# Kernel tuning notes

Measured on AMD Instinct MI355X. Metric: run time of the kernel, lower is better.

## Reference

```python
import jax, jax.numpy as jnp
import numpy as np
import math

H = 2048
NH = 16
NKV = 4
HD = H // NH  # 128
N_REP = NH // NKV
EPS = 1e-6


def rms_norm(x, w, eps=1e-6):
    x32 = x.astype(jnp.float32)
    y = x32 * jax.lax.rsqrt(jnp.mean(x32 * x32, axis=-1, keepdims=True) + eps)
    return (y * w.astype(jnp.float32)).astype(x.dtype)


def mha(normed, key_in, val_in, q_w, k_w, v_w, o_w, bias):
    # normed: [b,s,H]; key_in/val_in: [b,n,H]; bias broadcastable to [b,nh,s,n]
    b, s, _ = normed.shape
    n = key_in.shape[1]
    q = (normed @ q_w).reshape(b, s, NH, HD).transpose(0, 2, 1, 3)      # [b,nh,s,d]
    k = (key_in @ k_w).reshape(b, n, NKV, HD).transpose(0, 2, 1, 3)     # [b,nkv,n,d]
    v = (val_in @ v_w).reshape(b, n, NKV, HD).transpose(0, 2, 1, 3)
    k = jnp.repeat(k, N_REP, axis=1)  # GQA expand -> [b,nh,n,d]
    v = jnp.repeat(v, N_REP, axis=1)
    scores = jnp.einsum('bhsd,bhnd->bhsn', q, k) / math.sqrt(HD) + bias
    probs = jax.nn.softmax(scores.astype(jnp.float32), axis=-1).astype(q.dtype)
    out = jnp.einsum('bhsn,bhnd->bhsd', probs, v)
    out = out.transpose(0, 2, 1, 3).reshape(b, s, NH * HD) @ o_w
    return out, probs


def setup_inputs() -> dict:
    key = jax.random.key(0)
    ks = jax.random.split(key, 20)
    B, S, ND, T = 2, 2048, 64, 2048
    w = lambda k, sh: (jax.random.normal(k, sh, dtype=jnp.float32) * 0.02)
    return {
        'hidden_states': jax.random.normal(ks[0], (B, S, H), dtype=jnp.float32),
        'doc_summary_key': jax.random.normal(ks[1], (B, ND, H), dtype=jnp.float32),
        'doc_summary_value': jax.random.normal(ks[2], (B, ND, H), dtype=jnp.float32),
        'doc_summary_mask': jnp.ones((B, ND), dtype=jnp.float32),
        'token_key': jax.random.normal(ks[3], (B, T, H), dtype=jnp.float32),
        'token_value': jax.random.normal(ks[4], (B, T, H), dtype=jnp.float32),
        'token_mask': jnp.ones((B, T), dtype=jnp.float32),
        'cn_w': jnp.ones((H,), dtype=jnp.float32),
        'cq_w': w(ks[5], (H, NH * HD)),
        'ck_w': w(ks[6], (H, NKV * HD)),
        'cv_w': w(ks[7], (H, NKV * HD)),
        'co_w': w(ks[8], (NH * HD, H)),
        'c_gate': jnp.array([-1.0], dtype=jnp.float32),
        'fn_w': jnp.ones((H,), dtype=jnp.float32),
        'fq_w': w(ks[9], (H, NH * HD)),
        'fk_w': w(ks[10], (H, NKV * HD)),
        'fv_w': w(ks[11], (H, NKV * HD)),
        'fo_w': w(ks[12], (NH * HD, H)),
        'f_gate': jnp.array([-1.0], dtype=jnp.float32),
        'doc_token_map': jax.random.randint(ks[13], (B, T), 0, ND, dtype=jnp.int64)
            if jax.config.jax_enable_x64 else jax.random.randint(ks[13], (B, T), 0, ND).astype(jnp.int32),
    }


def reference(hidden_states, doc_summary_key, doc_summary_value, doc_summary_mask,
              token_key, token_value, token_mask,
              cn_w, cq_w, ck_w, cv_w, co_w, c_gate,
              fn_w, fq_w, fk_w, fv_w, fo_w, f_gate,
              doc_token_map):
    # ---- coarse stage: cross-attention over document summaries ----
    normed = rms_norm(hidden_states, cn_w)
    coarse_bias = ((1.0 - doc_summary_mask) * -1e9)[:, None, None, :]  # [b,1,1,nd]
    attn_out, probs = mha(normed, doc_summary_key, doc_summary_value,
                          cq_w, ck_w, cv_w, co_w, coarse_bias)
    doc_scores = probs.mean(axis=(1, 2))  # [b,nd] avg over heads+query positions
    gate_c = jax.nn.sigmoid(c_gate).astype(attn_out.dtype)
    out = hidden_states + gate_c * attn_out

    # ---- fine stage: cross-attention over token KV with log-doc-score bias ----
    log_ds = jnp.log(doc_scores + EPS)
    doc_bias = jnp.take_along_axis(log_ds, doc_token_map, axis=1)  # [b,T]
    pad_bias = (1.0 - token_mask) * -1e9
    fine_bias = (doc_bias + pad_bias)[:, None, None, :]  # [b,1,1,T]
    normed_f = rms_norm(out, fn_w)
    attn_out_f, _ = mha(normed_f, token_key, token_value,
                        fq_w, fk_w, fv_w, fo_w, fine_bias)
    gate_f = jax.nn.sigmoid(f_gate).astype(attn_out_f.dtype)
    final = out + gate_f * attn_out_f
    return final
```

## Files before the change

### kernel.cpp

```cpp
#include <hip/hip_runtime.h>
#include <hip/hip_bf16.h>

typedef unsigned short u16;
typedef unsigned int u32;
typedef __attribute__((ext_vector_type(8))) short bf16x8;
typedef __attribute__((ext_vector_type(4))) float f32x4;

constexpr int NH = 16;
constexpr int H = 2048;
constexpr float SCALE = 0.08838834764831845f;
constexpr float L2E = 1.4426950408889634f;
constexpr float SCALE2 = SCALE * L2E;
constexpr float THR2 = 8.0f * L2E;

__device__ __forceinline__ u16 f2bf(float f) {
    u32 u = __float_as_uint(f);
    u32 r = u + 0x7fffu + ((u >> 16) & 1u);
    return (u16)(r >> 16);
}
__device__ __forceinline__ u32 pack2(float x, float y) {
    return (u32)f2bf(x) | ((u32)f2bf(y) << 16);
}
__device__ __forceinline__ u32 pack2_cvt(float x, float y) {
    __hip_bfloat162 h = __float22bfloat162_rn(float2{x, y});
    return *reinterpret_cast<u32*>(&h);
}

#define GLD_LDS16(gsrc, ldst)                                                  \
    __builtin_amdgcn_global_load_lds(                                          \
        (const __attribute__((address_space(1))) void*)(gsrc),                 \
        (__attribute__((address_space(3))) void*)(ldst), 16, 0, 0)

__global__ __launch_bounds__(256)
void transpose_cvt4(const float* __restrict__ i0, const float* __restrict__ i1,
                    const float* __restrict__ i2, const float* __restrict__ i3,
                    u16* __restrict__ o0, u16* __restrict__ o1,
                    u16* __restrict__ o2, u16* __restrict__ o3, int K, int N) {
    const float* in = (blockIdx.z == 0) ? i0 : (blockIdx.z == 1) ? i1
                    : (blockIdx.z == 2) ? i2 : i3;
    u16* out = (blockIdx.z == 0) ? o0 : (blockIdx.z == 1) ? o1
             : (blockIdx.z == 2) ? o2 : o3;
    __shared__ u16 tile[32][33];
    int bn = blockIdx.x * 32, bk = blockIdx.y * 32;
    int tx = threadIdx.x & 31, ty = threadIdx.x >> 5;
#pragma unroll
    for (int r = 0; r < 32; r += 8)
        tile[tx][r + ty] = f2bf(in[(size_t)(bk + r + ty) * N + bn + tx]);
    __syncthreads();
#pragma unroll
    for (int r = 0; r < 32; r += 8)
        out[(size_t)(bn + r + ty) * K + bk + tx] = tile[r + ty][tx];
}

__global__ __launch_bounds__(256)
void rmsnorm_cvt(const float* __restrict__ x, const float* __restrict__ w,
                 u16* __restrict__ y, int nrows,
                 const float* __restrict__ ca, u16* __restrict__ coa,
                 const float* __restrict__ cb, u16* __restrict__ cob, int n4) {
    int blk = blockIdx.x;
    int t = threadIdx.x;
    if (blk >= nrows) {
        int nb = gridDim.x - nrows;
        int stride = nb * 256;
        for (int i = (blk - nrows) * 256 + t; i < 2 * n4; i += stride) {
            const float* in;
            u16* out;
            int j = i;
            if (j < n4) { in = ca; out = coa; }
            else { j -= n4; in = cb; out = cob; }
            float4 v = reinterpret_cast<const float4*>(in)[j];
            uint2 o;
            o.x = pack2(v.x, v.y);
            o.y = pack2(v.z, v.w);
            reinterpret_cast<uint2*>(out)[j] = o;
        }
        return;
    }
    int r = blk;
    const float4* xr = reinterpret_cast<const float4*>(x + (size_t)r * H);
    float4 v0 = xr[t * 2], v1 = xr[t * 2 + 1];
    float ss = v0.x * v0.x + v0.y * v0.y + v0.z * v0.z + v0.w * v0.w
             + v1.x * v1.x + v1.y * v1.y + v1.z * v1.z + v1.w * v1.w;
#pragma unroll
    for (int d = 1; d < 64; d <<= 1) ss += __shfl_xor(ss, d);
    __shared__ float red[4];
    if ((t & 63) == 0) red[t >> 6] = ss;
    __syncthreads();
    float tot = red[0] + red[1] + red[2] + red[3];
    float rs = rsqrtf(tot * (1.0f / H) + 1e-6f);
    const float4* wr = reinterpret_cast<const float4*>(w);
    float4 w0 = wr[t * 2], w1 = wr[t * 2 + 1];
    uint4 o;
    o.x = pack2(v0.x * rs * w0.x, v0.y * rs * w0.y);
    o.y = pack2(v0.z * rs * w0.z, v0.w * rs * w0.w);
    o.z = pack2(v1.x * rs * w1.x, v1.y * rs * w1.y);
    o.w = pack2(v1.z * rs * w1.z, v1.w * rs * w1.w);
    reinterpret_cast<uint4*>(y + (size_t)r * H)[t] = o;
}

template <int MODE, int BN>
__device__ __forceinline__
void gemm_body(u16* __restrict__ smem,
               const u16* __restrict__ A, const u16* __restrict__ Bt,
               u16* __restrict__ Cb, float* __restrict__ Cf,
               const float* __restrict__ resid, const float* __restrict__ gate_p,
               int N, int K, int brow, int bcol) {
    constexpr int WN = BN / 32;
    constexpr int BWROWS = BN / 4;
    u16* Asb = smem;
    u16* Bsb = smem + 2 * 128 * 64;
    const int t = threadIdx.x;
    const int lane = t & 63, wid = t >> 6;
    const int wm = wid >> 1, wn = wid & 1;
    const int l15 = lane & 15, hi = lane >> 4;
    const int rsw = l15 & 7;

    f32x4 acc[4][WN] = {};
    const int srow = lane >> 3;
    const int sseg = ((lane & 7) ^ srow) * 8;
    const u16* aBase = A + (size_t)(brow + wid * 32 + srow) * K + sseg;
    const u16* bBase = Bt + (size_t)(bcol + wid * BWROWS + srow) * K + sseg;

#define GSTAGE(KT, BF)                                                          \
    do {                                                                        \
        _Pragma("unroll")                                                       \
        for (int u = 0; u < 4; ++u)                                             \
            GLD_LDS16(aBase + (size_t)(u * 8) * K + (KT),                       \
                      Asb + (BF) * 8192 + (wid * 32 + u * 8) * 64);             \
        _Pragma("unroll")                                                       \
        for (int u = 0; u < BWROWS / 8; ++u)                                    \
            GLD_LDS16(bBase + (size_t)(u * 8) * K + (KT),                       \
                      Bsb + (BF) * (BN * 64) + (wid * BWROWS + u * 8) * 64);    \
    } while (0)

    GSTAGE(0, 0);
    __syncthreads();
    int buf = 0;
    for (int kt = 0; kt < K; kt += 64) {
        if (kt + 64 < K) GSTAGE(kt + 64, buf ^ 1);
        const u16* as = Asb + buf * 8192;
        const u16* bs = Bsb + buf * (BN * 64);
        bf16x8 af[4][2], bfr[WN][2];
#pragma unroll
        for (int i = 0; i < 4; ++i) {
            int row = wm * 64 + i * 16 + l15;
#pragma unroll
            for (int ko = 0; ko < 2; ++ko)
                af[i][ko] = *reinterpret_cast<const bf16x8*>(
                    &as[row * 64 + (((ko * 4 + hi) ^ rsw) * 8)]);
        }
#pragma unroll
        for (int j = 0; j < WN; ++j) {
            int row = wn * (BN / 2) + j * 16 + l15;
#pragma unroll
            for (int ko = 0; ko < 2; ++ko)
                bfr[j][ko] = *reinterpret_cast<const bf16x8*>(
                    &bs[row * 64 + (((ko * 4 + hi) ^ rsw) * 8)]);
        }
#pragma unroll
        for (int ko = 0; ko < 2; ++ko)
#pragma unroll
            for (int i = 0; i < 4; ++i)
#pragma unroll
                for (int j = 0; j < WN; ++j)
                    acc[i][j] = __builtin_amdgcn_mfma_f32_16x16x32_bf16(
                        af[i][ko], bfr[j][ko], acc[i][j], 0, 0, 0);
        __syncthreads();
        buf ^= 1;
    }
#undef GSTAGE

    float g = 0.f;
    if (MODE == 1) g = 1.0f / (1.0f + expf(-gate_p[0]));
    const int r0 = hi * 4, c0 = l15;
#pragma unroll
    for (int i = 0; i < 4; ++i) {
#pragma unroll
        for (int j = 0; j < WN; ++j) {
            int col = bcol + wn * (BN / 2) + j * 16 + c0;
#pragma unroll
            for (int r = 0; r < 4; ++r) {
                int row = brow + wm * 64 + i * 16 + r0 + r;
                float v = acc[i][j][r];
                if (MODE == 0) Cb[(size_t)row * N + col] = f2bf(v);
                else Cf[(size_t)row * N + col] = resid[(size_t)row * N + col] + g * v;
            }
        }
    }
}

template <int MODE, int BN>
__global__ __launch_bounds__(256)
void gemm_tn(const u16* __restrict__ A, const u16* __restrict__ Bt,
             u16* __restrict__ Cb, float* __restrict__ Cf,
             const float* __restrict__ resid, const float* __restrict__ gate_p,
             int M, int N, int K) {
    __shared__ u16 smem[16384 + BN * 128];
    int nbx = gridDim.x;
    int nwg = nbx * gridDim.y;
    int lin = blockIdx.y * nbx + blockIdx.x;
    if (!(nwg & 7)) { int q = nwg >> 3; lin = (lin & 7) * q + (lin >> 3); }
    gemm_body<MODE, BN>(smem, A, Bt, Cb, Cf, resid, gate_p, N, K,
                        (lin / nbx) * 128, (lin % nbx) * BN);
}

template <int MODE, int BN>
__global__ __launch_bounds__(256)
void gemm_tn_mega(const u16* __restrict__ A, const u16* __restrict__ Bt,
                  u16* __restrict__ Cb, float* __restrict__ Cf,
                  const float* __restrict__ resid, const float* __restrict__ gate_p,
                  int M, int N, int K,
                  const float* __restrict__ ca, u16* __restrict__ coa,
                  const float* __restrict__ cb2, u16* __restrict__ cob, int n4,
                  const u16* __restrict__ Ak, const u16* __restrict__ Bk,
                  u16* __restrict__ Ck,
                  const u16* __restrict__ Av, const u16* __restrict__ Bv,
                  u16* __restrict__ Cv) {
    __shared__ u16 smem[16384 + BN * 128];
    if (blockIdx.z == 1) {
        int nblk = gridDim.x * gridDim.y;
        int stride = nblk * 256;
        for (int i = (blockIdx.y * gridDim.x + blockIdx.x) * 256 + threadIdx.x;
             i < 2 * n4; i += stride) {
            const float* in;
            u16* out;
            int j = i;
            if (j < n4) { in = ca; out = coa; }
            else { j -= n4; in = cb2; out = cob; }
            float4 v = reinterpret_cast<const float4*>(in)[j];
            uint2 o;
            o.x = pack2(v.x, v.y);
            o.y = pack2(v.z, v.w);
            reinterpret_cast<uint2*>(out)[j] = o;
        }
        return;
    }
    if (blockIdx.z == 2) {
        int lin = blockIdx.y * gridDim.x + blockIdx.x;
        if (lin < 8)
            gemm_body<0, 64>(smem, Ak, Bk, Ck, nullptr, nullptr, nullptr,
                             512, K, 0, lin * 64);
        else if (lin < 16)
            gemm_body<0, 64>(smem, Av, Bv, Cv, nullptr, nullptr, nullptr,
                             512, K, 0, (lin - 8) * 64);
        return;
    }
    int nbx = gridDim.x;
    int nwg = nbx * gridDim.y;
    int lin = blockIdx.y * nbx + blockIdx.x;
    if (!(nwg & 7)) { int q = nwg >> 3; lin = (lin & 7) * q + (lin >> 3); }
    gemm_body<MODE, BN>(smem, A, Bt, Cb, Cf, resid, gate_p, N, K,
                        (lin / nbx) * 128, (lin % nbx) * BN);
}

template <int MODE, int BN>
__global__ __launch_bounds__(256)
void gemm_tn_bias(const u16* __restrict__ A, const u16* __restrict__ Bt,
                  u16* __restrict__ Cb, float* __restrict__ Cf,
                  const float* __restrict__ resid, const float* __restrict__ gate_p,
                  int M, int N, int K,
                  const float* __restrict__ doc_part, const int* __restrict__ map,
                  const float* __restrict__ tmask, float* __restrict__ bias) {
    __shared__ u16 smem[16384 + BN * 128];
    if (blockIdx.z == 1) {
        int lin = blockIdx.y * gridDim.x + blockIdx.x;
        if (lin >= 16) return;
        __shared__ float lg[128];
        int t = threadIdx.x;
        if (t < 128) {
            float s = 0.f;
#pragma unroll
            for (int i = 0; i < 8; ++i) s += doc_part[i * 128 + t];
            lg[t] = logf(s / 32768.0f + 1e-6f);
        }
        __syncthreads();
        int i = lin * 256 + t;
        if (i < 2 * 2048) {
            int b = i >> 11;
            bias[i] = (lg[b * 64 + map[i]] + (1.0f - tmask[i]) * -1e9f) * L2E;
        }
        return;
    }
    int nbx = gridDim.x;
    int nwg = nbx * gridDim.y;
    int lin = blockIdx.y * nbx + blockIdx.x;
    if (!(nwg & 7)) { int q = nwg >> 3; lin = (lin & 7) * q + (lin >> 3); }
    gemm_body<MODE, BN>(smem, A, Bt, Cb, Cf, resid, gate_p, N, K,
                        (lin / nbx) * 128, (lin % nbx) * BN);
}

__global__ __launch_bounds__(256)
void gemm_triple(const u16* __restrict__ Aq, const u16* __restrict__ Bq,
                 u16* __restrict__ Cq,
                 const u16* __restrict__ Ak, const u16* __restrict__ Bk,
                 u16* __restrict__ Ck,
                 const u16* __restrict__ Av, const u16* __restrict__ Bv,
                 u16* __restrict__ Cv, int K) {
    __shared__ u16 smem[32768];
    int lin = blockIdx.x;
    if (!(lin & 1)) {
        int l = lin >> 1;
        int q = 512 >> 3;
        l = (l & 7) * q + (l >> 3);
        gemm_body<0, 128>(smem, Aq, Bq, Cq, nullptr, nullptr, nullptr, 2048, K,
                          (l / 16) * 128, (l % 16) * 128);
    } else {
        int j = lin >> 1;
        if (j < 256) {
            int q = 256 >> 3;
            j = (j & 7) * q + (j >> 3);
            gemm_body<0, 64>(smem, Ak, Bk, Ck, nullptr, nullptr, nullptr, 512, K,
                             (j / 8) * 128, (j % 8) * 64);
        } else {
            j -= 256;
            int q = 256 >> 3;
            j = (j & 7) * q + (j >> 3);
            gemm_body<0, 64>(smem, Av, Bv, Cv, nullptr, nullptr, nullptr, 4096, K,
                             (j / 64) * 128, (j % 64) * 64);
        }
    }
}

__global__ __launch_bounds__(256)
void coarse_attn(const u16* __restrict__ q, const u16* __restrict__ kc,
                 const u16* __restrict__ vc, const float* __restrict__ mask,
                 float* __restrict__ doc_part, u16* __restrict__ attn_c) {
    constexpr int SC = 2048 / 64;
    int bid = blockIdx.x;
    int b = bid / (NH * SC);
    int rem = bid % (NH * SC);
    int h = rem / SC, sc = rem % SC;
    int kv = h >> 2;
    int t = threadIdx.x, lane = t & 63, wid = t >> 6;
    const int l15 = lane & 15, k0 = (lane >> 4) * 8;

    __shared__ u16 Kt[64 * 136];
    __shared__ u16 Vt[128 * 72];
    __shared__ u16 Pt[4][16 * 72];
    __shared__ float p_acc[64];

    {
        int n = t >> 2, s2 = t & 3;
        const u16* src = kc + (size_t)(b * 64 + n) * 512 + kv * 128;
#pragma unroll
        for (int u = 0; u < 4; ++u) {
            int sg = s2 + u * 4;
            *reinterpret_cast<uint4*>(&Kt[n * 136 + sg * 8]) =
                *reinterpret_cast<const uint4*>(src + sg * 8);
        }
    }
    {
        int n = t & 63, dblk = t >> 6;
        const u16* src = vc + (size_t)(b * 64 + n) * 512 + kv * 128 + dblk * 32;
#pragma unroll
        for (int u = 0; u < 4; ++u) {
            u16 tmp[8];
            *reinterpret_cast<uint4*>(tmp) = *reinterpret_cast<const uint4*>(src + u * 8);
#pragma unroll
            for (int e = 0; e < 8; ++e) Vt[(dblk * 32 + u * 8 + e) * 72 + n] = tmp[e];
        }
    }
    if (t < 64) p_acc[t] = 0.f;
    __syncthreads();

    int qrow = sc * 64 + wid * 16 + l15;
    const u16* qsrc = q + (size_t)(b * 2048 + qrow) * 2048 + h * 128;
    bf16x8 af[4];
#pragma unroll
    for (int kk = 0; kk < 4; ++kk)
        af[kk] = *reinterpret_cast<const bf16x8*>(qsrc + kk * 32 + k0);

    f32x4 sc4[4] = {};
#pragma unroll
    for (int kk = 0; kk < 4; ++kk)
#pragma unroll
        for (int j = 0; j < 4; ++j) {
            bf16x8 bfr = *reinterpret_cast<const bf16x8*>(&Kt[(j * 16 + l15) * 136 + kk * 32 + k0]);
            sc4[j] = __builtin_amdgcn_mfma_f32_16x16x32_bf16(af[kk], bfr, sc4[j], 0, 0, 0);
        }

    float s[4][4];
#pragma unroll
    for (int j = 0; j < 4; ++j) {
        float bia = (1.0f - mask[b * 64 + j * 16 + l15]) * (-1e9f * L2E);
#pragma unroll
        for (int r = 0; r < 4; ++r) s[j][r] = sc4[j][r] * SCALE2 + bia;
    }
    float m4[4], l4[4];
#pragma unroll
    for (int r = 0; r < 4; ++r) {
        float m = fmaxf(fmaxf(s[0][r], s[1][r]), fmaxf(s[2][r], s[3][r]));
#pragma unroll
        for (int d = 1; d < 16; d <<= 1) m = fmaxf(m, __shfl_xor(m, d));
        m4[r] = m;
    }
#pragma unroll
    for (int r = 0; r < 4; ++r) {
        float l = 0.f;
#pragma unroll
        for (int j = 0; j < 4; ++j) { s[j][r] = exp2f(s[j][r] - m4[r]); l += s[j][r]; }
#pragma unroll
        for (int d = 1; d < 16; d <<= 1) l += __shfl_xor(l, d);
        l4[r] = l;
    }
#pragma unroll
    for (int j = 0; j < 4; ++j) {
        float cs = 0.f;
#pragma unroll
        for (int r = 0; r < 4; ++r) {
            float pr = s[j][r] / l4[r];
            Pt[wid][((lane >> 4) * 4 + r) * 72 + j * 16 + l15] = f2bf(pr);
            cs += pr;
        }
        cs += __shfl_xor(cs, 16);
        cs += __shfl_xor(cs, 32);
        if (lane < 16) atomicAdd(&p_acc[j * 16 + lane], cs);
    }
    __syncthreads();

    f32x4 o4[8] = {};
#pragma unroll
    for (int kk2 = 0; kk2 < 2; ++kk2) {
        bf16x8 a2 = *reinterpret_cast<const bf16x8*>(&Pt[wid][l15 * 72 + kk2 * 32 + k0]);
#pragma unroll
        for (int j2 = 0; j2 < 8; ++j2) {
            bf16x8 b2 = *reinterpret_cast<const bf16x8*>(&Vt[(j2 * 16 + l15) * 72 + kk2 * 32 + k0]);
            o4[j2] = __builtin_amdgcn_mfma_f32_16x16x32_bf16(a2, b2, o4[j2], 0, 0, 0);
        }
    }
#pragma unroll
    for (int j2 = 0; j2 < 8; ++j2)
#pragma unroll
        for (int r = 0; r < 4; ++r) {
            int row = sc * 64 + wid * 16 + (lane >> 4) * 4 + r;
            attn_c[(size_t)(b * 2048 + row) * 2048 + h * 128 + j2 * 16 + l15] = f2bf(o4[j2][r]);
        }
    if (t < 64) atomicAdd(&doc_part[(blockIdx.x & 7) * 128 + b * 64 + t], p_acc[t]);
}

__global__ __launch_bounds__(256, 2)
void flash_attn(const u16* __restrict__ q, const u16* __restrict__ kf,
                const u16* __restrict__ vT, const float* __restrict__ bias,
                u16* __restrict__ attn_f) {
    int bid = blockIdx.x;
    int b = bid >> 8;
    int rem = bid & 255;
    int h = rem >> 4, sc = rem & 15;
    int kv = h >> 2;
    int t = threadIdx.x, lane = t & 63, wid = t >> 6;
    const int l15 = lane & 15, hi = lane >> 4;
    const int k0 = hi * 8;
    const int rswp = l15 & 7;

    __shared__ u16 Kt[2][64 * 128];
    __shared__ u16 Vt[2][128 * 64];
    __shared__ u16 Pt[4][32 * 64];

    bf16x8 qf4[2][4];
#pragma unroll
    for (int f = 0; f < 2; ++f) {
        int qrow = sc * 128 + wid * 32 + f * 16 + l15;
        const u16* qsrc = q + (size_t)(b * 2048 + qrow) * 2048 + h * 128;
#pragma unroll
        for (int kk = 0; kk < 4; ++kk)
            qf4[f][kk] = *reinterpret_cast<const bf16x8*>(qsrc + kk * 32 + k0);
    }

    const int krl = lane >> 4, kslot = lane & 15;
    const int vrl = lane >> 3, vslot = lane & 7;
    const u16* kbase = kf + (size_t)(b * 2048) * 512 + kv * 128;
    const u16* vbase = vT + (size_t)(kv * 128) * 4096 + b * 2048;
    const float* bbase = bias + b * 2048;

#define STAGE_K(TT, BF)                                                            \
    do {                                                                           \
        _Pragma("unroll")                                                          \
        for (int u = 0; u < 4; ++u) {                                              \
            int row = wid * 16 + u * 4 + krl;                                      \
            const u16* src = kbase + (size_t)((TT) + row) * 512                    \
                             + ((kslot ^ (row & 7)) * 8);                          \
            GLD_LDS16(src, &Kt[BF][(wid * 16 + u * 4) * 128]);                     \
        }                                                                          \
    } while (0)
#define STAGE_V(TT, BF)                                                            \
    do {                                                                           \
        _Pragma("unroll")                                                          \
        for (int u = 0; u < 4; ++u) {                                              \
            int row = wid * 32 + u * 8 + vrl;                                      \
            const u16* src = vbase + (size_t)row * 4096 + (TT)                     \
                             + ((vslot ^ (row & 7)) * 8);                          \
            GLD_LDS16(src, &Vt[BF][(wid * 32 + u * 8) * 64]);                      \
        }                                                                          \
    } while (0)

    float mstate[2] = {-1e30f, -1e30f}, lstate[2] = {0.f, 0.f};
    f32x4 o4[2][8] = {};

    STAGE_K(0, 0);
    STAGE_V(0, 0);
    __syncthreads();
    int par = 0;

    for (int t0 = 0; t0 < 2048; t0 += 64) {
        int t1 = (t0 + 64) & 2047;
        STAGE_K(t1, par ^ 1);
        STAGE_V(t1, par ^ 1);

        f32x4 st0[4] = {}, st1[4] = {};
        __builtin_amdgcn_s_setprio(1);
#pragma unroll
        for (int kk = 0; kk < 4; ++kk)
#pragma unroll
            for (int kb = 0; kb < 4; ++kb) {
                int row = kb * 16 + l15;
                bf16x8 kfrag = *reinterpret_cast<const bf16x8*>(
                    &Kt[par][row * 128 + (((kk * 4 + hi) ^ (row & 7)) * 8)]);
                st0[kb] = __builtin_amdgcn_mfma_f32_16x16x32_bf16(kfrag, qf4[0][kk], st0[kb], 0, 0, 0);
                st1[kb] = __builtin_amdgcn_mfma_f32_16x16x32_bf16(kfrag, qf4[1][kk], st1[kb], 0, 0, 0);
            }
        __builtin_amdgcn_s_setprio(0);

        float p[2][4][4];
        float pmax[2] = {-1e30f, -1e30f};
#pragma unroll
        for (int kb = 0; kb < 4; ++kb) {
            float4 b4 = *reinterpret_cast<const float4*>(bbase + t0 + kb * 16 + hi * 4);
            float bb[4] = {b4.x, b4.y, b4.z, b4.w};
#pragma unroll
            for (int r = 0; r < 4; ++r) {
                float v0 = st0[kb][r] * SCALE2 + bb[r];
                float v1 = st1[kb][r] * SCALE2 + bb[r];
                p[0][kb][r] = v0;
                p[1][kb][r] = v1;
                pmax[0] = fmaxf(pmax[0], v0);
                pmax[1] = fmaxf(pmax[1], v1);
            }
        }
#pragma unroll
        for (int f = 0; f < 2; ++f) {
            pmax[f] = fmaxf(pmax[f], __shfl_xor(pmax[f], 16));
            pmax[f] = fmaxf(pmax[f], __shfl_xor(pmax[f], 32));
        }

        bool need = (pmax[0] > mstate[0] + THR2) || (pmax[1] > mstate[1] + THR2);
        if (__any(need)) {
#pragma unroll
            for (int f = 0; f < 2; ++f) {
                float mnew = fmaxf(mstate[f], pmax[f]);
                float sco = exp2f(mstate[f] - mnew);
                float sco_out[4];
#pragma unroll
                for (int r = 0; r < 4; ++r) sco_out[r] = __shfl(sco, hi * 4 + r);
#pragma unroll
                for (int j2 = 0; j2 < 8; ++j2)
#pragma unroll
                    for (int r = 0; r < 4; ++r) o4[f][j2][r] *= sco_out[r];
                lstate[f] *= sco;
                mstate[f] = mnew;
            }
        }

#pragma unroll
        for (int f = 0; f < 2; ++f) {
            float lt = 0.f;
#pragma unroll
            for (int kb = 0; kb < 4; ++kb)
#pragma unroll
                for (int r = 0; r < 4; ++r) {
                    p[f][kb][r] = exp2f(p[f][kb][r] - mstate[f]);
                    lt += p[f][kb][r];
                }
            lt += __shfl_xor(lt, 16);
            lt += __shfl_xor(lt, 32);
            lstate[f] += lt;
        }

#pragma unroll
        for (int f = 0; f < 2; ++f)
#pragma unroll
            for (int kb = 0; kb < 4; ++kb) {
                uint2 w;
                w.x = pack2_cvt(p[f][kb][0], p[f][kb][1]);
                w.y = pack2_cvt(p[f][kb][2], p[f][kb][3]);
                int idx = (f * 16 + l15) * 64
                        + (((kb * 2 + (hi >> 1)) ^ rswp) * 8) + (hi & 1) * 4;
                *reinterpret_cast<uint2*>(&Pt[wid][idx]) = w;
            }

        __builtin_amdgcn_s_setprio(1);
#pragma unroll
        for (int kc2 = 0; kc2 < 2; ++kc2) {
            bf16x8 pa0 = *reinterpret_cast<const bf16x8*>(
                &Pt[wid][l15 * 64 + (((kc2 * 4 + hi) ^ rswp) * 8)]);
            bf16x8 pa1 = *reinterpret_cast<const bf16x8*>(
                &Pt[wid][(16 + l15) * 64 + (((kc2 * 4 + hi) ^ rswp) * 8)]);
#pragma unroll
            for (int j2 = 0; j2 < 8; ++j2) {
                int d = j2 * 16 + l15;
                bf16x8 vb = *reinterpret_cast<const bf16x8*>(
                    &Vt[par][d * 64 + (((kc2 * 4 + hi) ^ (d & 7)) * 8)]);
                o4[0][j2] = __builtin_amdgcn_mfma_f32_16x16x32_bf16(pa0, vb, o4[0][j2], 0, 0, 0);
                o4[1][j2] = __builtin_amdgcn_mfma_f32_16x16x32_bf16(pa1, vb, o4[1][j2], 0, 0, 0);
            }
        }
        __builtin_amdgcn_s_setprio(0);
        __syncthreads();
        par ^= 1;
    }
#undef STAGE_K
#undef STAGE_V

#pragma unroll
    for (int f = 0; f < 2; ++f) {
        float linv[4];
#pragma unroll
        for (int r = 0; r < 4; ++r) linv[r] = 1.0f / __shfl(lstate[f], hi * 4 + r);
#pragma unroll
        for (int j2 = 0; j2 < 8; ++j2)
#pragma unroll
            for (int r = 0; r < 4; ++r) {
                int row = sc * 128 + wid * 32 + f * 16 + hi * 4 + r;
                attn_f[(size_t)(b * 2048 + row) * 2048 + h * 128 + j2 * 16 + l15] =
                    f2bf(o4[f][j2][r] * linv[r]);
            }
    }
}

extern "C" void kernel_launch(void* const* d_in, const int* in_sizes, int n_in,
                              void* d_out, int out_size, void* d_ws, size_t ws_size,
                              hipStream_t stream) {
    const float* hidden = (const float*)d_in[0];
    const float* dsk    = (const float*)d_in[1];
    const float* dsv    = (const float*)d_in[2];
    const float* dsmask = (const float*)d_in[3];
    const float* tk     = (const float*)d_in[4];
    const float* tv     = (const float*)d_in[5];
    const float* tmask  = (const float*)d_in[6];
    const float* cn_w   = (const float*)d_in[7];
    const float* cq_w   = (const float*)d_in[8];
    const float* ck_w   = (const float*)d_in[9];
    const float* cv_w   = (const float*)d_in[10];
    const float* co_w   = (const float*)d_in[11];
    const float* c_gate = (const float*)d_in[12];
    const float* fn_w   = (const float*)d_in[13];
    const float* fq_w   = (const float*)d_in[14];
    const float* fk_w   = (const float*)d_in[15];
    const float* fv_w   = (const float*)d_in[16];
    const float* fo_w   = (const float*)d_in[17];
    const float* f_gate = (const float*)d_in[18];
    const int*   map    = (const int*)d_in[19];
    float* out_f = (float*)d_out;

    char* ws = (char*)d_ws;
    size_t off = 0;
    auto alloc = [&](size_t bytes) {
        char* p = ws + off;
        off += (bytes + 255) & ~(size_t)255;
        return p;
    };
    u16*  normA = (u16*)alloc(4096ULL * 2048 * 2);
    u16*  qbuf  = (u16*)alloc(4096ULL * 2048 * 2);
    u16*  kc    = (u16*)alloc(128ULL * 512 * 2);
    u16*  vc    = (u16*)alloc(128ULL * 512 * 2);
    u16*  kfb   = (u16*)alloc(4096ULL * 512 * 2);
    u16*  vTb   = (u16*)alloc(512ULL * 4096 * 2);
    u16*  tkb   = (u16*)alloc(4096ULL * 2048 * 2);
    u16*  tvb   = (u16*)alloc(4096ULL * 2048 * 2);
    u16*  dskb  = (u16*)alloc(128ULL * 2048 * 2);
    u16*  dsvb  = (u16*)alloc(128ULL * 2048 * 2);
    u16*  cqT   = (u16*)alloc(2048ULL * 2048 * 2);
    u16*  ckT   = (u16*)alloc(512ULL * 2048 * 2);
    u16*  cvT   = (u16*)alloc(512ULL * 2048 * 2);
    u16*  coT   = (u16*)alloc(2048ULL * 2048 * 2);
    u16*  fqT   = (u16*)alloc(2048ULL * 2048 * 2);
    u16*  fkT   = (u16*)alloc(512ULL * 2048 * 2);
    u16*  fvT   = (u16*)alloc(512ULL * 2048 * 2);
    u16*  foT   = (u16*)alloc(2048ULL * 2048 * 2);
    float* doc_part = (float*)alloc(8 * 128 * 4);
    float* biasb    = (float*)alloc(4096 * 4);

    hipMemsetAsync(doc_part, 0, 8 * 128 * 4, stream);

    transpose_cvt4<<<dim3(64, 64, 4), 256, 0, stream>>>(cq_w, co_w, fq_w, fo_w,
                                                        cqT, coT, fqT, foT, 2048, 2048);
    transpose_cvt4<<<dim3(16, 64, 4), 256, 0, stream>>>(ck_w, cv_w, fk_w, fv_w,
                                                        ckT, cvT, fkT, fvT, 2048, 512);

    rmsnorm_cvt<<<4096 + 256, 256, 0, stream>>>(hidden, cn_w, normA, 4096,
                                                dsk, dskb, dsv, dsvb, 128 * 2048 / 4);

    gemm_tn_mega<0, 128><<<dim3(16, 32, 3), 256, 0, stream>>>(
        normA, cqT, qbuf, nullptr, nullptr, nullptr, 4096, 2048, 2048,
        tk, tkb, tv, tvb, 4096 * 2048 / 4,
        dskb, ckT, kc, dsvb, cvT, vc);

    coarse_attn<<<1024, 256, 0, stream>>>(qbuf, kc, vc, dsmask, doc_part, normA);

    gemm_tn_bias<1, 128><<<dim3(16, 32, 2), 256, 0, stream>>>(
        normA, coT, nullptr, out_f, hidden, c_gate, 4096, 2048, 2048,
        doc_part, map, tmask, biasb);

    rmsnorm_cvt<<<4096, 256, 0, stream>>>(out_f, fn_w, qbuf, 4096,
                                          nullptr, nullptr, nullptr, nullptr, 0);
    gemm_triple<<<1024, 256, 0, stream>>>(qbuf, fqT, normA,
                                          tkb, fkT, kfb,
                                          fvT, tvb, vTb, 2048);

    flash_attn<<<512, 256, 0, stream>>>(normA, kfb, vTb, biasb, qbuf);

    gemm_tn<1, 128><<<dim3(16, 32), 256, 0, stream>>>(qbuf, foT, nullptr, out_f, out_f, f_gate, 4096, 2048, 2048);
}
```

Baseline: 403.4 us.

## Fold weight transposes into preamble and coarse-attention kernels to cut launches

```diff
diff --git a/kernel.cpp b/kernel.cpp
--- a/kernel.cpp
+++ b/kernel.cpp
@@ -31,17 +31,9 @@
         (const __attribute__((address_space(1))) void*)(gsrc),                 \
         (__attribute__((address_space(3))) void*)(ldst), 16, 0, 0)
 
-__global__ __launch_bounds__(256)
-void transpose_cvt4(const float* __restrict__ i0, const float* __restrict__ i1,
-                    const float* __restrict__ i2, const float* __restrict__ i3,
-                    u16* __restrict__ o0, u16* __restrict__ o1,
-                    u16* __restrict__ o2, u16* __restrict__ o3, int K, int N) {
-    const float* in = (blockIdx.z == 0) ? i0 : (blockIdx.z == 1) ? i1
-                    : (blockIdx.z == 2) ? i2 : i3;
-    u16* out = (blockIdx.z == 0) ? o0 : (blockIdx.z == 1) ? o1
-             : (blockIdx.z == 2) ? o2 : o3;
-    __shared__ u16 tile[32][33];
-    int bn = blockIdx.x * 32, bk = blockIdx.y * 32;
+__device__ __forceinline__
+void transpose_tile(const float* __restrict__ in, u16* __restrict__ out,
+                    int K, int N, int bn, int bk, u16 (*tile)[33]) {
     int tx = threadIdx.x & 31, ty = threadIdx.x >> 5;
 #pragma unroll
     for (int r = 0; r < 32; r += 8)
@@ -53,21 +45,48 @@
 }
 
 __global__ __launch_bounds__(256)
-void rmsnorm_cvt(const float* __restrict__ x, const float* __restrict__ w,
-                 u16* __restrict__ y, int nrows,
-                 const float* __restrict__ ca, u16* __restrict__ coa,
-                 const float* __restrict__ cb, u16* __restrict__ cob, int n4) {
+void preamble(const float* __restrict__ hidden, const float* __restrict__ cn_w,
+              u16* __restrict__ normA,
+              const float* __restrict__ dsk, u16* __restrict__ dskb,
+              const float* __restrict__ dsv, u16* __restrict__ dsvb,
+              const float* __restrict__ cq_w, u16* __restrict__ cqT,
+              const float* __restrict__ ck_w, u16* __restrict__ ckT,
+              const float* __restrict__ cv_w, u16* __restrict__ cvT) {
+    __shared__ u16 tile[32][33];
+    __shared__ float red[4];
     int blk = blockIdx.x;
     int t = threadIdx.x;
-    if (blk >= nrows) {
-        int nb = gridDim.x - nrows;
-        int stride = nb * 256;
-        for (int i = (blk - nrows) * 256 + t; i < 2 * n4; i += stride) {
+    if (blk < 4096) {
+        int r = blk;
+        const float4* xr = reinterpret_cast<const float4*>(hidden + (size_t)r * H);
+        float4 v0 = xr[t * 2], v1 = xr[t * 2 + 1];
+        float ss = v0.x * v0.x + v0.y * v0.y + v0.z * v0.z + v0.w * v0.w
+                 + v1.x * v1.x + v1.y * v1.y + v1.z * v1.z + v1.w * v1.w;
+#pragma unroll
+        for (int d = 1; d < 64; d <<= 1) ss += __shfl_xor(ss, d);
+        if ((t & 63) == 0) red[t >> 6] = ss;
+        __syncthreads();
+        float tot = red[0] + red[1] + red[2] + red[3];
+        float rs = rsqrtf(tot * (1.0f / H) + 1e-6f);
+        const float4* wr = reinterpret_cast<const float4*>(cn_w);
+        float4 w0 = wr[t * 2], w1 = wr[t * 2 + 1];
+        uint4 o;
+        o.x = pack2(v0.x * rs * w0.x, v0.y * rs * w0.y);
+        o.y = pack2(v0.z * rs * w0.z, v0.w * rs * w0.w);
+        o.z = pack2(v1.x * rs * w1.x, v1.y * rs * w1.y);
+        o.w = pack2(v1.z * rs * w1.z, v1.w * rs * w1.w);
+        reinterpret_cast<uint4*>(normA + (size_t)r * H)[t] = o;
+        return;
+    }
+    if (blk < 4352) {
+        const int n4 = 128 * 2048 / 4;
+        int stride = 256 * 256;
+        for (int i = (blk - 4096) * 256 + t; i < 2 * n4; i += stride) {
             const float* in;
             u16* out;
             int j = i;
-            if (j < n4) { in = ca; out = coa; }
-            else { j -= n4; in = cb; out = cob; }
+            if (j < n4) { in = dsk; out = dskb; }
+            else { j -= n4; in = dsv; out = dsvb; }
             float4 v = reinterpret_cast<const float4*>(in)[j];
             uint2 o;
             o.x = pack2(v.x, v.y);
@@ -76,7 +95,22 @@
         }
         return;
     }
-    int r = blk;
+    int r = blk - 4352;
+    if (r < 4096) {
+        transpose_tile(cq_w, cqT, 2048, 2048, (r & 63) * 32, (r >> 6) * 32, tile);
+    } else {
+        r -= 4096;
+        int m = r >> 10, rr = r & 1023;
+        transpose_tile(m ? cv_w : ck_w, m ? cvT : ckT, 2048, 512,
+                       (rr & 15) * 32, (rr >> 4) * 32, tile);
+    }
+}
+
+__global__ __launch_bounds__(256)
+void rmsnorm_kernel(const float* __restrict__ x, const float* __restrict__ w,
+                    u16* __restrict__ y) {
+    int r = blockIdx.x;
+    int t = threadIdx.x;
     const float4* xr = reinterpret_cast<const float4*>(x + (size_t)r * H);
     float4 v0 = xr[t * 2], v1 = xr[t * 2 + 1];
     float ss = v0.x * v0.x + v0.y * v0.y + v0.z * v0.z + v0.w * v0.w
@@ -322,11 +356,32 @@
 }
 
 __global__ __launch_bounds__(256)
-void coarse_attn(const u16* __restrict__ q, const u16* __restrict__ kc,
-                 const u16* __restrict__ vc, const float* __restrict__ mask,
-                 float* __restrict__ doc_part, u16* __restrict__ attn_c) {
+void coarse_attn_tr(const u16* __restrict__ q, const u16* __restrict__ kc,
+                    const u16* __restrict__ vc, const float* __restrict__ mask,
+                    float* __restrict__ doc_part, u16* __restrict__ attn_c,
+                    const float* __restrict__ co_w, u16* __restrict__ coT,
+                    const float* __restrict__ fq_w, u16* __restrict__ fqT,
+                    const float* __restrict__ fo_w, u16* __restrict__ foT,
+                    const float* __restrict__ fk_w, u16* __restrict__ fkT,
+                    const float* __restrict__ fv_w, u16* __restrict__ fvT) {
+    __shared__ u16 tile[32][33];
+    int bid = blockIdx.x;
+    if (bid >= 1024) {
+        int r = bid - 1024;
+        if (r < 12288) {
+            int m = r / 4096, rr = r % 4096;
+            const float* in = (m == 0) ? co_w : (m == 1) ? fq_w : fo_w;
+            u16* out = (m == 0) ? coT : (m == 1) ? fqT : foT;
+            transpose_tile(in, out, 2048, 2048, (rr & 63) * 32, (rr >> 6) * 32, tile);
+        } else {
+            int r2 = r - 12288;
+            int m = r2 >> 10, rr = r2 & 1023;
+            transpose_tile(m ? fv_w : fk_w, m ? fvT : fkT, 2048, 512,
+                           (rr & 15) * 32, (rr >> 4) * 32, tile);
+        }
+        return;
+    }
     constexpr int SC = 2048 / 64;
-    int bid = blockIdx.x;
     int b = bid / (NH * SC);
     int rem = bid % (NH * SC);
     int h = rem / SC, sc = rem % SC;
@@ -435,7 +490,7 @@
             int row = sc * 64 + wid * 16 + (lane >> 4) * 4 + r;
             attn_c[(size_t)(b * 2048 + row) * 2048 + h * 128 + j2 * 16 + l15] = f2bf(o4[j2][r]);
         }
-    if (t < 64) atomicAdd(&doc_part[(blockIdx.x & 7) * 128 + b * 64 + t], p_acc[t]);
+    if (t < 64) atomicAdd(&doc_part[(bid & 7) * 128 + b * 64 + t], p_acc[t]);
 }
 
 __global__ __launch_bounds__(256, 2)
@@ -681,27 +736,24 @@
 
     hipMemsetAsync(doc_part, 0, 8 * 128 * 4, stream);
 
-    transpose_cvt4<<<dim3(64, 64, 4), 256, 0, stream>>>(cq_w, co_w, fq_w, fo_w,
-                                                        cqT, coT, fqT, foT, 2048, 2048);
-    transpose_cvt4<<<dim3(16, 64, 4), 256, 0, stream>>>(ck_w, cv_w, fk_w, fv_w,
-                                                        ckT, cvT, fkT, fvT, 2048, 512);
-
-    rmsnorm_cvt<<<4096 + 256, 256, 0, stream>>>(hidden, cn_w, normA, 4096,
-                                                dsk, dskb, dsv, dsvb, 128 * 2048 / 4);
+    preamble<<<10496, 256, 0, stream>>>(hidden, cn_w, normA,
+                                        dsk, dskb, dsv, dsvb,
+                                        cq_w, cqT, ck_w, ckT, cv_w, cvT);
 
     gemm_tn_mega<0, 128><<<dim3(16, 32, 3), 256, 0, stream>>>(
         normA, cqT, qbuf, nullptr, nullptr, nullptr, 4096, 2048, 2048,
         tk, tkb, tv, tvb, 4096 * 2048 / 4,
         dskb, ckT, kc, dsvb, cvT, vc);
 
-    coarse_attn<<<1024, 256, 0, stream>>>(qbuf, kc, vc, dsmask, doc_part, normA);
+    coarse_attn_tr<<<15360, 256, 0, stream>>>(qbuf, kc, vc, dsmask, doc_part, normA,
+                                              co_w, coT, fq_w, fqT, fo_w, foT,
+                                              fk_w, fkT, fv_w, fvT);
 
     gemm_tn_bias<1, 128><<<dim3(16, 32, 2), 256, 0, stream>>>(
         normA, coT, nullptr, out_f, hidden, c_gate, 4096, 2048, 2048,
         doc_part, map, tmask, biasb);
 
-    rmsnorm_cvt<<<4096, 256, 0, stream>>>(out_f, fn_w, qbuf, 4096,
-                                          nullptr, nullptr, nullptr, nullptr, 0);
+    rmsnorm_kernel<<<4096, 256, 0, stream>>>(out_f, fn_w, qbuf);
     gemm_triple<<<1024, 256, 0, stream>>>(qbuf, fqT, normA,
                                           tkb, fkT, kfb,
                                           fvT, tvb, vTb, 2048);
```

Result: no change. 400.5 us (-0.7%).
